# Kernel tuning notes

Hardware: AMD Instinct MI355X
Metric: run time of the kernel (lower is better)

## Reference

```python
import jax, jax.numpy as jnp
import numpy as np

NUM_WORDS = 10000
IN_DIM = 300
SIZE = 256
NUM_SEQ = 2
B = 16
L = 128
NUM_BASE_LEMMAS = 3000


def _lstm(x, Wi, Wh, b):
    # x: [L, B, D] -> hidden states [L, B, H]
    Bb = x.shape[1]
    H = Wh.shape[0]
    def step(carry, xt):
        h, c = carry
        z = xt @ Wi + h @ Wh + b  # [B, 4H], gate order i,f,g,o (torch convention)
        i, f, g, o = jnp.split(z, 4, axis=-1)
        c = jax.nn.sigmoid(f) * c + jax.nn.sigmoid(i) * jnp.tanh(g)
        h = jax.nn.sigmoid(o) * jnp.tanh(c)
        return (h, c), h
    init = (jnp.zeros((Bb, H), x.dtype), jnp.zeros((Bb, H), x.dtype))
    _, hs = jax.lax.scan(step, init, x)
    return hs


def _bilstm(x, lengths, Wi_f, Wh_f, b_f, Wi_b, Wh_b, b_b):
    # x: [B, L, D]; variable-length bidirectional LSTM, concat outputs [B, L, 2H]
    Bb, Ll, _ = x.shape
    t = jnp.arange(Ll)
    # reverse the valid prefix of each row; padding stays in place
    rev_idx = jnp.where(t[None, :] < lengths[:, None], lengths[:, None] - 1 - t[None, :], t[None, :])
    x_rev = jnp.take_along_axis(x, rev_idx[:, :, None], axis=1)
    hf = _lstm(jnp.swapaxes(x, 0, 1), Wi_f, Wh_f, b_f)
    hb = _lstm(jnp.swapaxes(x_rev, 0, 1), Wi_b, Wh_b, b_b)
    hf = jnp.swapaxes(hf, 0, 1)
    hb = jnp.take_along_axis(jnp.swapaxes(hb, 0, 1), rev_idx[:, :, None], axis=1)
    return jnp.concatenate([hf, hb], axis=-1)


def setup_inputs() -> dict:
    key = jax.random.key(0)
    ks = jax.random.split(key, 16)
    d = {}
    d['word_embeddings'] = jax.random.normal(ks[0], (NUM_WORDS, IN_DIM), jnp.float32)
    # embedding projection Linear(IN_DIM, SIZE)
    d['Wp'] = jax.random.normal(ks[1], (IN_DIM, SIZE), jnp.float32) * 0.05
    d['bp'] = jnp.zeros((SIZE,), jnp.float32)
    D = SIZE + NUM_SEQ
    d['Wi_f'] = jax.random.normal(ks[2], (D, 4 * SIZE), jnp.float32) * 0.05
    d['Wh_f'] = jax.random.normal(ks[3], (SIZE, 4 * SIZE), jnp.float32) * 0.05
    d['b_f'] = jnp.zeros((4 * SIZE,), jnp.float32)
    d['Wi_b'] = jax.random.normal(ks[4], (D, 4 * SIZE), jnp.float32) * 0.05
    d['Wh_b'] = jax.random.normal(ks[5], (SIZE, 4 * SIZE), jnp.float32) * 0.05
    d['b_b'] = jnp.zeros((4 * SIZE,), jnp.float32)
    # encoded projection Linear(2*SIZE, SIZE)
    d['Wenc'] = jax.random.normal(ks[6], (2 * SIZE, SIZE), jnp.float32) * 0.05
    d['benc'] = jnp.zeros((SIZE,), jnp.float32)
    # gate projection Linear(2*SIZE, SIZE), bias init 1.0 per source
    d['Wgate'] = jax.random.normal(ks[7], (2 * SIZE, SIZE), jnp.float32) * 0.05
    d['bgate'] = jnp.ones((SIZE,), jnp.float32)
    d['seq0'] = jax.random.randint(ks[8], (B, L), 0, NUM_WORDS, jnp.int32)
    d['seq1'] = jax.random.randint(ks[9], (B, L), 0, NUM_WORDS, jnp.int32)
    d['len0'] = jax.random.randint(ks[10], (B,), 1, L + 1, jnp.int32)
    d['len1'] = jax.random.randint(ks[11], (B,), 1, L + 1, jnp.int32)
    d['u2l'] = jax.random.randint(ks[12], (NUM_WORDS,), 0, NUM_BASE_LEMMAS, jnp.int32)
    return d


def reference(word_embeddings, Wp, bp, Wi_f, Wh_f, b_f, Wi_b, Wh_b, b_b, Wenc, benc, Wgate, bgate, seq0, seq1, len0, len1, u2l):
    num_words = word_embeddings.shape[0]
    batch = seq0.shape[0]
    size = Wp.shape[1]
    we = jax.nn.relu(word_embeddings @ Wp + bp)  # [num_words, size]
    offsets = jnp.arange(batch, dtype=jnp.int32) * num_words  # [B]
    u2l_off = (u2l[None, :] + offsets[:, None]).reshape(-1)  # [B*num_words]
    num_lemmas = batch * num_words
    ctxt = jnp.tile(we, (batch, 1))  # [B*num_words, size]
    for i, (seq, lengths) in enumerate(((seq0, len0), (seq1, len1))):
        Ll = seq.shape[1]
        seq_off = seq + offsets[:, None]  # [B, L]
        enc_in = ctxt[seq_off]  # gather: [B, L, size]
        mode = jnp.zeros((batch, Ll, NUM_SEQ), enc_in.dtype).at[:, :, i].set(1.0)
        enc_in = jnp.concatenate([enc_in, mode], axis=-1)  # [B, L, size+num_seq]
        h = _bilstm(enc_in, lengths, Wi_f, Wh_f, b_f, Wi_b, Wh_b, b_b)  # [B, L, 2*size]
        enc = h @ Wenc + benc  # [B, L, size]
        mask = (jnp.arange(Ll)[None, :] < lengths[:, None]).astype(enc.dtype)
        enc = enc * mask[:, :, None]
        seq_lemmas = u2l_off[seq_off.reshape(-1)]  # [B*L]
        new_lemma = jax.ops.segment_max(enc.reshape(-1, size), seq_lemmas, num_segments=num_lemmas)
        new_lemma = jax.nn.relu(new_lemma)  # empty segments (-inf) -> 0
        new_word = new_lemma[u2l_off]  # scatter-back via gather: [B*num_words, size]
        gate = jax.nn.sigmoid(jnp.concatenate([ctxt, new_word], axis=-1) @ Wgate + bgate)
        ctxt = ctxt * gate + (1.0 - gate) * new_word
    return ctxt
```

## Files before the change

### kernel.cpp

```cpp
#include <hip/hip_runtime.h>

#define NW    10000
#define INDIM 300
#define SZ    256
#define BB    16
#define LL    128
#define NLEM  3000
#define FH    1024
#define NCAP  8192
#define NB1   157

typedef short  bf16x8 __attribute__((ext_vector_type(8)));
typedef float  f32x4  __attribute__((ext_vector_type(4)));

__device__ __forceinline__ float sigf(float x){
  return __builtin_amdgcn_rcpf(1.f+__builtin_amdgcn_exp2f(-1.442695041f*x));
}
__device__ __forceinline__ float tanhf_(float x){
  return fmaf(-2.f, __builtin_amdgcn_rcpf(1.f+__builtin_amdgcn_exp2f(2.885390082f*x)), 1.f);
}
__device__ __forceinline__ short f2b(float f){
  unsigned u=__float_as_uint(f); u += 0x7FFFu + ((u>>16)&1u); return (short)(u>>16);
}
__device__ __forceinline__ int pack2(float a, float b){
  return ((int)(unsigned short)f2b(a)) | (((int)(unsigned short)f2b(b))<<16);
}
#define B2F(s) __uint_as_float(((unsigned)(unsigned short)(s))<<16)
#define MFA(a,b,c) __builtin_amdgcn_mfma_f32_16x16x32_bf16(a,b,c,0,0,0)

__global__ void k_prepall(const float* __restrict__ Wh_f, const float* __restrict__ Wh_b,
                          short* __restrict__ whb,
                          const float* __restrict__ Wi_f, const float* __restrict__ Wi_b,
                          short* __restrict__ wif,
                          const float* __restrict__ Wenc, short* __restrict__ wef,
                          const float* __restrict__ Wp, short* __restrict__ wpf){
  int bx=blockIdx.x, thr=threadIdx.x;
  if(bx<256){
    int tid=bx*256+thr;
    int l=tid&63, f=(tid>>6)&63, w=(tid>>12)&7, dir=tid>>15;
    const float* Wh = dir? Wh_b : Wh_f;
    int ks=f&7, T2=f>>3, s2=T2>>2, g=T2&3;
    int col = g*256 + w*32 + s2*16 + (l&15);
    int k0  = ks*32 + (l>>4)*8;
    short v[8];
    #pragma unroll
    for(int j=0;j<8;j++) v[j]=f2b(Wh[(long)(k0+j)*FH + col]);
    *(bf16x8*)(whb + (long)tid*8) = *(bf16x8*)v;
  }else if(bx<512){
    int tid=(bx-256)*256+thr;
    int l=tid&63, ks=(tid>>6)&7, ct=(tid>>9)&63, dir=tid>>15;
    const float* Wi = dir? Wi_b : Wi_f;
    int col = ct*16 + (l&15);
    int k0  = ks*32 + (l>>4)*8;
    short v[8];
    #pragma unroll
    for(int j=0;j<8;j++) v[j]=f2b(Wi[(long)(k0+j)*FH + col]);
    *(bf16x8*)(wif + (long)tid*8) = *(bf16x8*)v;
  }else if(bx<576){
    int tid=(bx-512)*256+thr;
    int l=tid&63, ks=(tid>>6)&15, ct=tid>>10;
    int col = ct*16 + (l&15);
    int k0  = ks*32 + (l>>4)*8;
    short v[8];
    #pragma unroll
    for(int j=0;j<8;j++) v[j]=f2b(Wenc[(long)(k0+j)*SZ + col]);
    *(bf16x8*)(wef + (long)tid*8) = *(bf16x8*)v;
  }else{
    int tid2=(bx-576)*256+thr;
    int l=tid2&63, frow=tid2>>6;
    int ct=frow/10, ks=frow-ct*10;
    int col=ct*16+(l&15);
    int k0=ks*32+(l>>4)*8;
    short v[8];
    #pragma unroll
    for(int j=0;j<8;j++){ int k=k0+j; v[j]=(k<INDIM)? f2b(Wp[(long)k*SZ+col]) : (short)0; }
    *(bf16x8*)(wpf + (long)frow*512 + l*8) = *(bf16x8*)v;
  }
}

__global__ void k_we_mfma(const float* __restrict__ emb, const short* __restrict__ wpf,
                          const float* __restrict__ bp, float* __restrict__ we){
  __shared__ __align__(16) short As[64*328];
  int r0=blockIdx.x*64, tid=threadIdx.x, w=tid>>6, l=tid&63;
  for(int i=tid;i<64*160;i+=256){
    int lr=i/160, c2=(i-lr*160)*2;
    int row=r0+lr;
    float e0=0.f,e1=0.f;
    if(row<NW){
      if(c2<INDIM)   e0=emb[(long)row*INDIM+c2];
      if(c2+1<INDIM) e1=emb[(long)row*INDIM+c2+1];
    }
    *(int*)&As[lr*328+c2]=pack2(e0,e1);
  }
  __syncthreads();
  for(int n2=0;n2<4;n2++){
    int ct=w*4+n2;
    f32x4 Z={0.f,0.f,0.f,0.f};
    f32x4 C0=Z,C1=Z,C2=Z,C3=Z;
    #pragma unroll
    for(int ks=0;ks<10;ks++){
      bf16x8 bb=*(const bf16x8*)(wpf+((long)(ct*10+ks))*512+l*8);
      int ao=ks*32+(l>>4)*8;
      bf16x8 a0=*(const bf16x8*)(&As[((l&15)    )*328+ao]);
      bf16x8 a1=*(const bf16x8*)(&As[((l&15)+16 )*328+ao]);
      bf16x8 a2=*(const bf16x8*)(&As[((l&15)+32 )*328+ao]);
      bf16x8 a3=*(const bf16x8*)(&As[((l&15)+48 )*328+ao]);
      C0=MFA(a0,bb,C0); C1=MFA(a1,bb,C1); C2=MFA(a2,bb,C2); C3=MFA(a3,bb,C3);
    }
    int col=ct*16+(l&15);
    float be=bp[col];
    #pragma unroll
    for(int m=0;m<4;m++){
      f32x4 Cm=(m==0)?C0:(m==1)?C1:(m==2)?C2:C3;
      #pragma unroll
      for(int reg=0;reg<4;reg++){
        int row=r0+m*16+(l>>4)*4+reg;
        if(row<NW) we[(long)row*SZ+col]=fmaxf(Cm[reg]+be,0.f);
      }
    }
  }
}

__global__ void k_xwi_mfma(const int* __restrict__ seq, const int* __restrict__ len,
                      const float* __restrict__ srcw, long bstride,
                      const float* __restrict__ ctxtT, const int* __restrict__ idxmap,
                      const float* __restrict__ Wi_f, const float* __restrict__ bvf,
                      const float* __restrict__ Wi_b, const float* __restrict__ bvb,
                      const short* __restrict__ wf, int iseq, short* __restrict__ xwo){
  __shared__ __align__(16) short As[64*264];
  __shared__ const float* rowp[64];
  int bx=blockIdx.x, dir=bx>>5, blk=bx&31, tid=threadIdx.x;
  int w=tid>>6, l=tid&63;
  if(tid<64){
    int t = blk*4 + (tid>>4), b = tid&15;
    int lb=len[b];
    int tt=(dir==0)? t : ((t<lb)? (lb-1-t) : t);
    int tok=seq[b*LL+tt];
    const float* rp;
    if(idxmap){
      int im=idxmap[b*NW+tok];
      rp = (im>=0)? ctxtT+(long)im*SZ : srcw+(long)tok*SZ;
    }else{
      rp = srcw + (long)b*bstride + (long)tok*SZ;
    }
    rowp[tid]=rp;
  }
  __syncthreads();
  for(int i2=tid;i2<64*64;i2+=256){
    int lr=i2>>6, c4=(i2&63)*4;
    float4 v=*(const float4*)(rowp[lr]+c4);
    int2 pk; pk.x=pack2(v.x,v.y); pk.y=pack2(v.z,v.w);
    *(int2*)&As[lr*264+c4]=pk;
  }
  __syncthreads();
  const float* __restrict__ Wi = dir? Wi_b : Wi_f;
  const float* __restrict__ bv = dir? bvb : bvf;
  const short* wfd = wf + (long)dir*262144;
  for(int n2=0;n2<16;n2++){
    int ct = w*16 + n2;
    const short* bfp = wfd + ((long)ct*8)*512 + l*8;
    f32x4 Z={0.f,0.f,0.f,0.f};
    f32x4 C0=Z,C1=Z,C2=Z,C3=Z;
    #pragma unroll
    for(int ks=0;ks<8;ks++){
      bf16x8 bb=*(const bf16x8*)(bfp + ks*512);
      int ao = ks*32 + (l>>4)*8;
      bf16x8 a0=*(const bf16x8*)(&As[((l&15)    )*264 + ao]);
      bf16x8 a1=*(const bf16x8*)(&As[((l&15)+16 )*264 + ao]);
      bf16x8 a2=*(const bf16x8*)(&As[((l&15)+32 )*264 + ao]);
      bf16x8 a3=*(const bf16x8*)(&As[((l&15)+48 )*264 + ao]);
      C0=MFA(a0,bb,C0); C1=MFA(a1,bb,C1); C2=MFA(a2,bb,C2); C3=MFA(a3,bb,C3);
    }
    int g=ct>>4, w2=(ct&15)>>1, s2=ct&1;
    int col = g*256 + w2*32 + s2*16 + (l&15);
    float be = Wi[(long)(SZ+iseq)*FH+col] + bv[col];
    #pragma unroll
    for(int m=0;m<4;m++){
      f32x4 Cm = (m==0)?C0:(m==1)?C1:(m==2)?C2:C3;
      long base=((((long)dir*128 + blk*4 + m)*8 + w2)*64 + (l>>4)*16 + (l&15))*32
                + s2*16 + g*4;
      int2 pk; pk.x=pack2(Cm[0]+be,Cm[1]+be); pk.y=pack2(Cm[2]+be,Cm[3]+be);
      *(int2*)(xwo+base)=pk;
    }
  }
}

__device__ __forceinline__ void rowgemm64(const float* __restrict__ A,
                                          const float* __restrict__ W,
                                          float* __restrict__ C,
                                          int n, int r0, int tid, float* Asf){
  for(int i=tid;i<64*SZ;i+=512){
    int lr=i>>8; int r=r0+lr;
    Asf[i]= (r<n)? A[(long)r*SZ+(i&255)] : 0.f;
  }
  __syncthreads();
  int cl=tid&63, rg=tid>>6;
  float acc[8][4];
  #pragma unroll
  for(int i=0;i<8;i++){acc[i][0]=acc[i][1]=acc[i][2]=acc[i][3]=0.f;}
  for(int k=0;k<SZ;k+=4){
    float4 a4[8];
    #pragma unroll
    for(int i=0;i<8;i++) a4[i]=*(const float4*)&Asf[(rg*8+i)*SZ+k];
    #pragma unroll
    for(int j=0;j<4;j++){
      const float* wr=W+(long)(k+j)*SZ+cl;
      float w0=wr[0],w1=wr[64],w2=wr[128],w3=wr[192];
      #pragma unroll
      for(int i=0;i<8;i++){
        float a=(j==0)?a4[i].x:(j==1)?a4[i].y:(j==2)?a4[i].z:a4[i].w;
        acc[i][0]=fmaf(a,w0,acc[i][0]);acc[i][1]=fmaf(a,w1,acc[i][1]);
        acc[i][2]=fmaf(a,w2,acc[i][2]);acc[i][3]=fmaf(a,w3,acc[i][3]);
      }
    }
  }
  #pragma unroll
  for(int i=0;i<8;i++){
    int r=r0+rg*8+i;
    if(r<n){
      #pragma unroll
      for(int cc=0;cc<4;cc++) C[(long)r*SZ+cl+cc*64]=acc[i][cc];
    }
  }
}

#define LDFW(f)    (*(const bf16x8*)(fr + (long)(f)*512 + l*8))
#define LDLW(i2,ks) (*(const bf16x8*)(bl + ((i2)*8+(ks))*512 + l*8))
#define DECLWT(T) bf16x8 W##T##_0=LDFW((T)*8+0),W##T##_1=LDFW((T)*8+1),W##T##_2=LDFW((T)*8+2),W##T##_3=LDFW((T)*8+3),W##T##_4=LDFW((T)*8+4),W##T##_5=LDFW((T)*8+5),W##T##_6=LDFW((T)*8+6),W##T##_7=LDFW((T)*8+7);
#define MMRT(T,Cv) { Cv=MFA(A0,W##T##_0,Cv); Cv=MFA(A1,W##T##_1,Cv); Cv=MFA(A2,W##T##_2,Cv); Cv=MFA(A3,W##T##_3,Cv); Cv=MFA(A4,W##T##_4,Cv); Cv=MFA(A5,W##T##_5,Cv); Cv=MFA(A6,W##T##_6,Cv); Cv=MFA(A7,W##T##_7,Cv); }
#define MMLT(i2,Cv) { Cv=MFA(A0,LDLW(i2,0),Cv); Cv=MFA(A1,LDLW(i2,1),Cv); Cv=MFA(A2,LDLW(i2,2),Cv); Cv=MFA(A3,LDLW(i2,3),Cv); Cv=MFA(A4,LDLW(i2,4),Cv); Cv=MFA(A5,LDLW(i2,5),Cv); Cv=MFA(A6,LDLW(i2,6),Cv); Cv=MFA(A7,LDLW(i2,7),Cv); }
#define MMST(Cv) { Cv=MFA(A0,S0,Cv); Cv=MFA(A1,S1,Cv); Cv=MFA(A2,S2,Cv); Cv=MFA(A3,S3,Cv); Cv=MFA(A4,S4,Cv); Cv=MFA(A5,S5,Cv); Cv=MFA(A6,S6,Cv); Cv=MFA(A7,S7,Cv); }
#define LOADST(f0) S0=LDFW((f0)+0); S1=LDFW((f0)+1); S2=LDFW((f0)+2); S3=LDFW((f0)+3); S4=LDFW((f0)+4); S5=LDFW((f0)+5); S6=LDFW((f0)+6); S7=LDFW((f0)+7);
#define G1(s,r,CA,CB,CC,CD,XA,XB) { \
  float zi=CA[r]+B2F(XA[r]), zf=CB[r]+B2F(XA[4+(r)]), zg=CC[r]+B2F(XB[r]), zo=CD[r]+B2F(XB[4+(r)]); \
  cst_##s##_##r = sigf(zf)*cst_##s##_##r + sigf(zi)*tanhf_(zg); \
  float hv = sigf(zo)*tanhf_(cst_##s##_##r); \
  int b_=4*(l>>4)+(r); int u_=w*32+(s)*16+(l&15); \
  hbn[b_*264+u_]=f2b(hv); }
#define GP(s,CA,CB,CC,CD,XA,XB) \
  G1(s,0,CA,CB,CC,CD,XA,XB) G1(s,1,CA,CB,CC,CD,XA,XB) \
  G1(s,2,CA,CB,CC,CD,XA,XB) G1(s,3,CA,CB,CC,CD,XA,XB)

extern __shared__ char smem_raw[];

__global__ __launch_bounds__(512,2) void k_lstm_f(
    const short* __restrict__ frag, const short* __restrict__ xq,
    short* __restrict__ hgs,
    const float* __restrict__ gA1, const float* __restrict__ gW1,
    float* __restrict__ gC1, int n1,
    const float* __restrict__ gA2, const float* __restrict__ gW2,
    float* __restrict__ gC2, const int* __restrict__ cnt2, int ncap2,
    const int* __restrict__ zsA, const int* __restrict__ zsB,
    const int* __restrict__ u2l, float* __restrict__ lemz,
    int* __restrict__ flagz, int* __restrict__ cntz){
  const int bid=blockIdx.x, tid=threadIdx.x;
  if(bid>=2){
    int gb=bid-2;
    float* Asf=(float*)smem_raw;
    int nb1 = gA1 ? (n1+63)>>6 : 0;
    if(gb<nb1){ rowgemm64(gA1,gW1,gC1,n1,gb*64,tid,Asf); return; }
    gb-=nb1;
    int nb2 = gA2 ? (ncap2>>6) : 0;
    if(gb<nb2){
      int n2=*cnt2; if(n2>ncap2)n2=ncap2;
      int r0=gb*64;
      if(r0<n2) rowgemm64(gA2,gW2,gC2,n2,r0,tid,Asf);
      return;
    }
    gb-=nb2;
    if(zsA){
      if(gb<256){
        int r8=gb*8+(tid>>6); int b=r8>>7, t=r8&127;
        int lem=u2l[zsA[b*LL+t]];
        *(float4*)(lemz+((long)b*NLEM+lem)*SZ+(tid&63)*4)=make_float4(0.f,0.f,0.f,0.f);
        return;
      }
      gb-=256;
    }
    if(zsB){
      if(gb<256){
        int r8=gb*8+(tid>>6); int b=r8>>7, t=r8&127;
        int lem=u2l[zsB[b*LL+t]];
        *(float4*)(lemz+((long)b*NLEM+lem)*SZ+(tid&63)*4)=make_float4(0.f,0.f,0.f,0.f);
        return;
      }
      gb-=256;
    }
    {
      int idx=gb*512+tid;
      if(idx<12000) ((int4*)flagz)[idx]=make_int4(0,0,0,0);
      if(cntz && gb==0 && tid==0) *cntz=0;
    }
    return;
  }
  const int dir=bid, w=tid>>6, l=tid&63;
  short* hb=(short*)smem_raw;
  short* bl=(short*)(smem_raw+16896)+w*8192;
  const short* fr = frag + (long)(dir*8+w)*32768;
  for(int i=tid;i<4224;i+=512) ((int*)smem_raw)[i]=0;
  #pragma unroll
  for(int c2=0;c2<16;c2++)
    *(f32x4*)(bl+c2*512+l*8) = *(const f32x4*)(fr+(long)(32+c2)*512+l*8);
  DECLWT(0) DECLWT(1) DECLWT(2) DECLWT(3)
  float cst_0_0=0,cst_0_1=0,cst_0_2=0,cst_0_3=0,
        cst_1_0=0,cst_1_1=0,cst_1_2=0,cst_1_3=0;
  __syncthreads();
  const short* xwb = xq + ((long)dir*128*8 + w)*2048 + (long)l*32;
  short* hgb = hgs + (long)dir*524288;
  const int db=tid>>5, du=(tid&31)*8;
  bf16x8 S0,S1,S2,S3,S4,S5,S6,S7;
  for(int t=0;t<LL;t++){
    const int cur=t&1, nxt=cur^1;
    LOADST(48)
    const short* xp = xwb + (long)t*16384;
    bf16x8 X0=*(const bf16x8*)(xp+0), X1=*(const bf16x8*)(xp+8);
    const short* hr = hb + cur*4224 + (l&15)*264 + (l>>4)*8;
    bf16x8 A0=*(const bf16x8*)(hr+0),   A1=*(const bf16x8*)(hr+32),
           A2=*(const bf16x8*)(hr+64),  A3=*(const bf16x8*)(hr+96),
           A4=*(const bf16x8*)(hr+128), A5=*(const bf16x8*)(hr+160),
           A6=*(const bf16x8*)(hr+192), A7=*(const bf16x8*)(hr+224);
    f32x4 Z={0.f,0.f,0.f,0.f};
    f32x4 C00=Z,C01=Z,C02=Z,C03=Z,C10=Z,C11=Z,C12=Z,C13=Z;
    MMRT(0,C00) MMRT(1,C01) MMRT(2,C02) MMRT(3,C03)
    MMLT(0,C10) MMLT(1,C11)
    MMST(C12)
    LOADST(56)
    bf16x8 X2=*(const bf16x8*)(xp+16), X3=*(const bf16x8*)(xp+24);
    short* hbn = hb + nxt*4224;
    GP(0, C00,C01,C02,C03, X0,X1)
    MMST(C13)
    GP(1, C10,C11,C12,C13, X2,X3)
    __syncthreads();
    f32x4 hv4 = *(const f32x4*)(hbn + db*264 + du);
    *(f32x4*)(hgb + ((long)t*16 + db)*256 + du) = hv4;
  }
}

__global__ void k_enc_mfma(const int* __restrict__ seq, const int* __restrict__ len,
                      const int* __restrict__ u2l, const short* __restrict__ hgs,
                      const short* __restrict__ wef, const float* __restrict__ benc,
                      unsigned int* __restrict__ lembuf, unsigned int* __restrict__ flags){
  __shared__ __align__(16) short As[64*520];
  __shared__ const short* pf16[64]; __shared__ const short* pb16[64];
  __shared__ int lem_s[64], val_s[64], b_s[64];
  int r0=blockIdx.x*64, tid=threadIdx.x, w=tid>>6, l=tid&63;
  if(tid<64){
    int r=r0+tid, b=r>>7, t=r&127, lb=len[b];
    int v=(t<lb); val_s[tid]=v; b_s[tid]=b;
    int lem=u2l[seq[r]]; lem_s[tid]=lem;
    pf16[tid]=hgs+((long)t*BB+b)*SZ;
    int tr=v? (lb-1-t) : t;
    pb16[tid]=hgs+((long)(LL+tr)*BB+b)*SZ;
    if(v) flags[(long)b*NLEM+lem]=1u;
  }
  __syncthreads();
  for(int i2=tid;i2<64*128;i2+=256){
    int lr=i2>>7, cc=(i2&127)*4;
    const short* sp=(cc<256)? pf16[lr]+cc : pb16[lr]+(cc-256);
    *(int2*)&As[lr*520+cc]=*(const int2*)sp;
  }
  __syncthreads();
  for(int n2=0;n2<4;n2++){
    int ct=w*4+n2;
    f32x4 Z={0.f,0.f,0.f,0.f};
    f32x4 C0=Z,C1=Z,C2=Z,C3=Z;
    #pragma unroll
    for(int ks=0;ks<16;ks++){
      bf16x8 bb=*(const bf16x8*)(wef+((long)(ct*16+ks))*512+l*8);
      int ao=ks*32+(l>>4)*8;
      bf16x8 a0=*(const bf16x8*)(&As[((l&15)    )*520+ao]);
      bf16x8 a1=*(const bf16x8*)(&As[((l&15)+16 )*520+ao]);
      bf16x8 a2=*(const bf16x8*)(&As[((l&15)+32 )*520+ao]);
      bf16x8 a3=*(const bf16x8*)(&As[((l&15)+48 )*520+ao]);
      C0=MFA(a0,bb,C0); C1=MFA(a1,bb,C1); C2=MFA(a2,bb,C2); C3=MFA(a3,bb,C3);
    }
    int col=ct*16+(l&15);
    float be=benc[col];
    #pragma unroll
    for(int m=0;m<4;m++){
      f32x4 Cm=(m==0)?C0:(m==1)?C1:(m==2)?C2:C3;
      #pragma unroll
      for(int reg=0;reg<4;reg++){
        int row=m*16+(l>>4)*4+reg;
        if(val_s[row]){
          float e=fmaxf(Cm[reg]+be,0.f);
          atomicMax(&lembuf[((long)b_s[row]*NLEM+lem_s[row])*SZ+col], __float_as_uint(e));
        }
      }
    }
  }
}

__global__ void k_rowgemm(const float* __restrict__ A, const float* __restrict__ W,
                          float* __restrict__ C, const unsigned int* __restrict__ flags){
  __shared__ __align__(16) float As[16][SZ];
  __shared__ int any_s;
  int r0=blockIdx.x*16, tid=threadIdx.x;
  if(tid==0){
    int a = flags? 0 : 1;
    if(flags){ for(int i=0;i<16;i++) a |= (int)flags[r0+i]; }
    any_s=a;
  }
  __syncthreads();
  if(!any_s) return;
  for(int i=tid;i<16*SZ;i+=256){int lr=i>>8,j=i&(SZ-1);As[lr][j]=A[(long)(r0+lr)*SZ+j];}
  __syncthreads();
  int cl=tid&63, rg=tid>>6;
  float acc[4][4];
  #pragma unroll
  for(int i=0;i<4;i++){acc[i][0]=acc[i][1]=acc[i][2]=acc[i][3]=0.f;}
  for(int k=0;k<SZ;k+=4){
    float4 a4[4];
    #pragma unroll
    for(int i=0;i<4;i++) a4[i]=*(const float4*)&As[rg*4+i][k];
    #pragma unroll
    for(int j=0;j<4;j++){
      const float* wr=W+(long)(k+j)*SZ+cl;
      float w0=wr[0],w1=wr[64],w2=wr[128],w3=wr[192];
      #pragma unroll
      for(int i=0;i<4;i++){
        float a=(j==0)?a4[i].x:(j==1)?a4[i].y:(j==2)?a4[i].z:a4[i].w;
        acc[i][0]=fmaf(a,w0,acc[i][0]);acc[i][1]=fmaf(a,w1,acc[i][1]);
        acc[i][2]=fmaf(a,w2,acc[i][2]);acc[i][3]=fmaf(a,w3,acc[i][3]);
      }
    }
  }
  #pragma unroll
  for(int i=0;i<4;i++){
    int r=r0+rg*4+i;
    #pragma unroll
    for(int cc=0;cc<4;cc++) C[(long)r*SZ+cl+cc*64]=acc[i][cc];
  }
}

__global__ void k_compact(const int* __restrict__ u2l, const unsigned int* __restrict__ flags,
                          int* __restrict__ cnt, int* __restrict__ list,
                          int* __restrict__ idxmap, int ncap){
  int r = blockIdx.x*256+threadIdx.x;
  if(r>=BB*NW) return;
  int b=r/NW, w=r-b*NW;
  int im=-1;
  if(flags[(long)b*NLEM+u2l[w]]){
    int idx=atomicAdd(cnt,1);
    if(idx<ncap){ list[idx]=r; im=idx; }
  }
  idxmap[r]=im;
}

__global__ void k_gate0c(const float* __restrict__ we, const float* __restrict__ P0,
                         const float* __restrict__ Q, const float* __restrict__ lembuf,
                         const int* __restrict__ u2l, const float* __restrict__ bg,
                         const int* __restrict__ cnt, const int* __restrict__ list,
                         float* __restrict__ ctxtT, int ncap){
  int n=*cnt; if(n>ncap)n=ncap;
  long idx=(long)blockIdx.x*256+threadIdx.x;
  long i=idx>>6; int k4=(int)(idx&63);
  if(i>=n) return;
  int r=list[i]; int b=r/NW, w=r-b*NW;
  int lem=u2l[w];
  long qb=((long)b*NLEM+lem)*SZ;
  float4 p =((const float4*)(P0+(long)w*SZ))[k4];
  float4 wv=((const float4*)(we+(long)w*SZ))[k4];
  float4 bgv=((const float4*)bg)[k4];
  float4 q =((const float4*)(Q+qb))[k4];
  float4 nw=((const float4*)(lembuf+qb))[k4];
  float4 o;
  { float g=sigf(p.x+q.x+bgv.x); o.x=wv.x*g+(1.f-g)*nw.x; }
  { float g=sigf(p.y+q.y+bgv.y); o.y=wv.y*g+(1.f-g)*nw.y; }
  { float g=sigf(p.z+q.z+bgv.z); o.z=wv.z*g+(1.f-g)*nw.z; }
  { float g=sigf(p.w+q.w+bgv.w); o.w=wv.w*g+(1.f-g)*nw.w; }
  ((float4*)ctxtT)[i*64+k4]=o;
}

__global__ void k_base0ip(float* __restrict__ we, const float* __restrict__ P0,
                          const float* __restrict__ bg){
  long idx=(long)blockIdx.x*256+threadIdx.x;
  if(idx>=(long)NW*SZ/4) return;
  int k4=(int)(idx&63);
  float4 wv=((float4*)we)[idx];
  float4 p =((const float4*)P0)[idx];
  float4 bgv=((const float4*)bg)[k4];
  wv.x*=sigf(p.x+bgv.x); wv.y*=sigf(p.y+bgv.y);
  wv.z*=sigf(p.z+bgv.z); wv.w*=sigf(p.w+bgv.w);
  ((float4*)we)[idx]=wv;
}

__global__ void k_gate0(const float* __restrict__ we, const float* __restrict__ P0,
                        const float* __restrict__ Q, const float* __restrict__ lembuf,
                        const int* __restrict__ u2l, const unsigned int* __restrict__ flags,
                        const float* __restrict__ bg, float* __restrict__ out){
  long idx=(long)blockIdx.x*256+threadIdx.x;
  const long TOTAL4=(long)BB*NW*SZ/4;
  if(idx>=TOTAL4) return;
  long row=idx>>6; int k4=(int)(idx&63);
  int r32=(int)row;
  int b=r32/NW, w=r32-b*NW;
  int lem=u2l[w];
  long qb=((long)b*NLEM+lem)*SZ;
  unsigned int fl=flags[(long)b*NLEM+lem];
  float4 p =((const float4*)(P0+(long)w*SZ))[k4];
  float4 wv=((const float4*)(we+(long)w*SZ))[k4];
  float4 bgv=((const float4*)bg)[k4];
  float4 q, nw;
  if(fl){ q=((const float4*)(Q+qb))[k4]; nw=((const float4*)(lembuf+qb))[k4]; }
  else  { q=make_float4(0.f,0.f,0.f,0.f); nw=q; }
  float4 o;
  { float g=sigf(p.x+q.x+bgv.x); o.x=wv.x*g+(1.f-g)*nw.x; }
  { float g=sigf(p.y+q.y+bgv.y); o.y=wv.y*g+(1.f-g)*nw.y; }
  { float g=sigf(p.z+q.z+bgv.z); o.z=wv.z*g+(1.f-g)*nw.z; }
  { float g=sigf(p.w+q.w+bgv.w); o.w=wv.w*g+(1.f-g)*nw.w; }
  ((float4*)out)[idx]=o;
}

__global__ void k_gate1e(const float* __restrict__ base0, const float* __restrict__ ctxtT,
                         const float* __restrict__ P1b, const float* __restrict__ Pt,
                         const int* __restrict__ idxmap,
                         const float* __restrict__ Q, const float* __restrict__ lembuf,
                         const int* __restrict__ u2l, const unsigned int* __restrict__ flags,
                         const float* __restrict__ bg, float* __restrict__ out){
  long idx=(long)blockIdx.x*256+threadIdx.x;
  const long TOTAL4=(long)BB*NW*SZ/4;
  if(idx>=TOTAL4) return;
  long row=idx>>6; int k4=(int)(idx&63);
  int r32=(int)row;
  int b=r32/NW, w=r32-b*NW;
  int im=idxmap[r32];
  int lem=u2l[w];
  long qb=((long)b*NLEM+lem)*SZ;
  unsigned int fl=flags[(long)b*NLEM+lem];
  float4 p, cv;
  if(im>=0){ p=((const float4*)(Pt+(long)im*SZ))[k4]; cv=((const float4*)(ctxtT+(long)im*SZ))[k4]; }
  else     { p=((const float4*)(P1b+(long)w*SZ))[k4]; cv=((const float4*)(base0+(long)w*SZ))[k4]; }
  float4 bgv=((const float4*)bg)[k4];
  float4 q, nw;
  if(fl){ q=((const float4*)(Q+qb))[k4]; nw=((const float4*)(lembuf+qb))[k4]; }
  else  { q=make_float4(0.f,0.f,0.f,0.f); nw=q; }
  float4 o;
  { float g=sigf(p.x+q.x+bgv.x); o.x=cv.x*g+(1.f-g)*nw.x; }
  { float g=sigf(p.y+q.y+bgv.y); o.y=cv.y*g+(1.f-g)*nw.y; }
  { float g=sigf(p.z+q.z+bgv.z); o.z=cv.z*g+(1.f-g)*nw.z; }
  { float g=sigf(p.w+q.w+bgv.w); o.w=cv.w*g+(1.f-g)*nw.w; }
  ((float4*)out)[idx]=o;
}

__global__ void k_gate1(const float* __restrict__ ctxt, const float* __restrict__ Wg,
                        const float* __restrict__ Q, const float* __restrict__ lembuf,
                        const int* __restrict__ u2l, const unsigned int* __restrict__ flags,
                        const float* __restrict__ bg, float* __restrict__ out){
  __shared__ __align__(16) float As[64][SZ];
  __shared__ __align__(16) float Ws[64][SZ];
  __shared__ int lem_s[64];
  int r0=blockIdx.x*64, tid=threadIdx.x;
  for(int i=tid;i<64*SZ;i+=256){int lr=i>>8,j=i&(SZ-1);
    As[lr][j]=ctxt[(long)(r0+lr)*SZ+j];}
  if(tid<64){int r=r0+tid; lem_s[tid]=u2l[r%NW];}
  int cl=tid&63, rg=tid>>6;
  float acc[16][4];
  #pragma unroll
  for(int i=0;i<16;i++){acc[i][0]=acc[i][1]=acc[i][2]=acc[i][3]=0.f;}
  for(int kb=0;kb<4;kb++){
    __syncthreads();
    for(int i=tid;i<64*SZ;i+=256){int lr=i>>8,j=i&(SZ-1);
      Ws[lr][j]=Wg[(long)(kb*64+lr)*SZ+j];}
    __syncthreads();
    for(int k=0;k<64;k+=4){
      float4 a4[16];
      #pragma unroll
      for(int i=0;i<16;i++) a4[i]=*(const float4*)&As[rg*16+i][kb*64+k];
      #pragma unroll
      for(int j=0;j<4;j++){
        float w0=Ws[k+j][cl],w1=Ws[k+j][cl+64],w2=Ws[k+j][cl+128],w3=Ws[k+j][cl+192];
        #pragma unroll
        for(int i=0;i<16;i++){
          float a=(j==0)?a4[i].x:(j==1)?a4[i].y:(j==2)?a4[i].z:a4[i].w;
          acc[i][0]=fmaf(a,w0,acc[i][0]);acc[i][1]=fmaf(a,w1,acc[i][1]);
          acc[i][2]=fmaf(a,w2,acc[i][2]);acc[i][3]=fmaf(a,w3,acc[i][3]);
        }
      }
    }
  }
  #pragma unroll
  for(int i=0;i<16;i++){
    int lr=rg*16+i, r=r0+lr, b=r/NW;
    long base=((long)b*NLEM+lem_s[lr])*SZ;
    unsigned int fl=flags[(long)b*NLEM+lem_s[lr]];
    #pragma unroll
    for(int cc=0;cc<4;cc++){
      int col=cl+cc*64;
      float qv=0.f, nw=0.f;
      if(fl){ qv=Q[base+col]; nw=lembuf[base+col]; }
      float g=sigf(acc[i][cc]+qv+bg[col]);
      out[(long)r*SZ+col]=As[lr][col]*g+(1.f-g)*nw;
    }
  }
}

extern "C" void kernel_launch(void* const* d_in, const int* in_sizes, int n_in,
                              void* d_out, int out_size, void* d_ws, size_t ws_size,
                              hipStream_t stream){
  const float* emb  =(const float*)d_in[0];
  const float* Wp   =(const float*)d_in[1];
  const float* bp   =(const float*)d_in[2];
  const float* Wi_f =(const float*)d_in[3];
  const float* Wh_f =(const float*)d_in[4];
  const float* b_f  =(const float*)d_in[5];
  const float* Wi_b =(const float*)d_in[6];
  const float* Wh_b =(const float*)d_in[7];
  const float* b_b  =(const float*)d_in[8];
  const float* Wenc =(const float*)d_in[9];
  const float* benc =(const float*)d_in[10];
  const float* Wg   =(const float*)d_in[11];
  const float* bg   =(const float*)d_in[12];
  const int*   seq0 =(const int*)d_in[13];
  const int*   seq1 =(const int*)d_in[14];
  const int*   len0 =(const int*)d_in[15];
  const int*   len1 =(const int*)d_in[16];
  const int*   u2l  =(const int*)d_in[17];

  float* ws    = (float*)d_ws;
  float* we    = ws;
  float* xwi   = we    + 2560000;
  float* ctxtT = xwi   + 2097152;
  float* hglob = xwi   + 4194304;
  float* lembuf= hglob + 1048576;
  float* flags = lembuf+ 12288000;
  float* Q     = flags + 48000;
  float* P0    = Q     + 12288000;
  short* whb   = (short*)(P0 + 2560000);
  short* wifrag= whb + 524288;
  short* wefrag= wifrag + 524288;
  short* wpfrag= wefrag + 131072;
  int*   idxmap= (int*)(P0 + 2560000 + 262144 + 262144 + 65536 + 40960);
  int*   list  = idxmap + 160000;
  int*   cnt   = list + NCAP;
  float* Ptouch= (float*)(cnt + 4);
  long base_floats = (long)(Ptouch - ws);
  long avail = ((long)(ws_size/4) - base_floats)/SZ;
  int sparse_ok = (avail >= NCAP);
  float* out   = (float*)d_out;

  hipFuncSetAttribute((const void*)k_lstm_f,
                      hipFuncAttributeMaxDynamicSharedMemorySize, 147968);

  k_prepall<<<616,256,0,stream>>>(Wh_f,Wh_b,whb, Wi_f,Wi_b,wifrag,
                                  Wenc,wefrag, Wp,wpfrag);
  k_we_mfma<<<NB1,256,0,stream>>>(emb,wpfrag,bp,we);

  k_xwi_mfma<<<64,256,0,stream>>>(seq0,len0,we,0L,nullptr,nullptr,
                                  Wi_f,b_f,Wi_b,b_b,wifrag,0,(short*)xwi);
  k_lstm_f<<<2+NB1+256+24,512,147968,stream>>>(whb,(const short*)xwi,(short*)hglob,
      we,Wg,P0,NW, nullptr,nullptr,nullptr,nullptr,0,
      seq0,nullptr,u2l,lembuf,(int*)flags,cnt);
  k_enc_mfma<<<BB*LL/64,256,0,stream>>>(seq0,len0,u2l,(const short*)hglob,wefrag,benc,
                                        (unsigned int*)lembuf,(unsigned int*)flags);
  k_rowgemm<<<BB*NLEM/16,256,0,stream>>>(lembuf,Wg+(long)SZ*SZ,Q,
                                         (const unsigned int*)flags);
  if(sparse_ok){
    k_compact<<<(BB*NW+255)/256,256,0,stream>>>(u2l,(const unsigned int*)flags,
                                                cnt,list,idxmap,NCAP);
    k_gate0c<<<NCAP*64/256,256,0,stream>>>(we,P0,Q,lembuf,u2l,bg,cnt,list,ctxtT,NCAP);
    k_base0ip<<<(NW*SZ/4+255)/256,256,0,stream>>>(we,P0,bg);
  }else{
    long nb=((long)BB*NW*SZ/4+255)/256;
    k_gate0<<<(int)nb,256,0,stream>>>(we,P0,Q,lembuf,u2l,
                                      (const unsigned int*)flags,bg,out);
  }

  if(sparse_ok){
    k_xwi_mfma<<<64,256,0,stream>>>(seq1,len1,we,0L,ctxtT,idxmap,
                                    Wi_f,b_f,Wi_b,b_b,wifrag,1,(short*)xwi);
    k_lstm_f<<<2+NB1+NCAP/64+256+256+24,512,147968,stream>>>(whb,(const short*)xwi,
        (short*)hglob, we,Wg,P0,NW, ctxtT,Wg,Ptouch,cnt,NCAP,
        seq0,seq1,u2l,lembuf,(int*)flags,nullptr);
  }else{
    k_xwi_mfma<<<64,256,0,stream>>>(seq1,len1,out,(long)NW*SZ,nullptr,nullptr,
                                    Wi_f,b_f,Wi_b,b_b,wifrag,1,(short*)xwi);
    k_lstm_f<<<2+256+256+24,512,147968,stream>>>(whb,(const short*)xwi,(short*)hglob,
        nullptr,nullptr,nullptr,0, nullptr,nullptr,nullptr,nullptr,0,
        seq0,seq1,u2l,lembuf,(int*)flags,nullptr);
  }
  k_enc_mfma<<<BB*LL/64,256,0,stream>>>(seq1,len1,u2l,(const short*)hglob,wefrag,benc,
                                        (unsigned int*)lembuf,(unsigned int*)flags);
  k_rowgemm<<<BB*NLEM/16,256,0,stream>>>(lembuf,Wg+(long)SZ*SZ,Q,
                                         (const unsigned int*)flags);
  if(sparse_ok){
    long nb=((long)BB*NW*SZ/4+255)/256;
    k_gate1e<<<(int)nb,256,0,stream>>>(we,ctxtT,P0,Ptouch,idxmap,Q,lembuf,u2l,
                                       (const unsigned int*)flags,bg,out);
  }else{
    k_gate1<<<BB*NW/64,256,0,stream>>>(out,Wg,Q,lembuf,u2l,
                                       (const unsigned int*)flags,bg,out);
  }
}
```

Measured before the change: 1.261 ms.

## Compact touched lemmas into a list and fuse Q gemm with word compaction

```diff
diff --git a/kernel.cpp b/kernel.cpp
--- a/kernel.cpp
+++ b/kernel.cpp
@@ -9,6 +9,7 @@
 #define FH    1024
 #define NCAP  8192
 #define NB1   157
+#define LEMCAP 4096
 
 typedef short  bf16x8 __attribute__((ext_vector_type(8)));
 typedef float  f32x4  __attribute__((ext_vector_type(4)));
@@ -252,7 +253,7 @@
     float* __restrict__ gC2, const int* __restrict__ cnt2, int ncap2,
     const int* __restrict__ zsA, const int* __restrict__ zsB,
     const int* __restrict__ u2l, float* __restrict__ lemz,
-    int* __restrict__ flagz, int* __restrict__ cntz){
+    int* __restrict__ flagz, int* __restrict__ cntz, int* __restrict__ lemcntz){
   const int bid=blockIdx.x, tid=threadIdx.x;
   if(bid>=2){
     int gb=bid-2;
@@ -289,7 +290,8 @@
     {
       int idx=gb*512+tid;
       if(idx<12000) ((int4*)flagz)[idx]=make_int4(0,0,0,0);
-      if(cntz && gb==0 && tid==0) *cntz=0;
+      if(gb==0 && tid==0 && cntz) *cntz=0;
+      if(gb==0 && tid==1 && lemcntz) *lemcntz=0;
     }
     return;
   }
@@ -339,7 +341,8 @@
 __global__ void k_enc_mfma(const int* __restrict__ seq, const int* __restrict__ len,
                       const int* __restrict__ u2l, const short* __restrict__ hgs,
                       const short* __restrict__ wef, const float* __restrict__ benc,
-                      unsigned int* __restrict__ lembuf, unsigned int* __restrict__ flags){
+                      unsigned int* __restrict__ lembuf, unsigned int* __restrict__ flags,
+                      int* __restrict__ lemcnt, int* __restrict__ lemlist){
   __shared__ __align__(16) short As[64*520];
   __shared__ const short* pf16[64]; __shared__ const short* pb16[64];
   __shared__ int lem_s[64], val_s[64], b_s[64];
@@ -351,7 +354,13 @@
     pf16[tid]=hgs+((long)t*BB+b)*SZ;
     int tr=v? (lb-1-t) : t;
     pb16[tid]=hgs+((long)(LL+tr)*BB+b)*SZ;
-    if(v) flags[(long)b*NLEM+lem]=1u;
+    if(v){
+      int fi=b*NLEM+lem;
+      if(atomicExch(&flags[fi],1u)==0u){
+        int pos=atomicAdd(lemcnt,1);
+        if(pos<LEMCAP) lemlist[pos]=fi;
+      }
+    }
   }
   __syncthreads();
   for(int i2=tid;i2<64*128;i2+=256){
@@ -391,19 +400,19 @@
   }
 }
 
-__global__ void k_rowgemm(const float* __restrict__ A, const float* __restrict__ W,
-                          float* __restrict__ C, const unsigned int* __restrict__ flags){
-  __shared__ __align__(16) float As[16][SZ];
-  __shared__ int any_s;
-  int r0=blockIdx.x*16, tid=threadIdx.x;
-  if(tid==0){
-    int a = flags? 0 : 1;
-    if(flags){ for(int i=0;i<16;i++) a |= (int)flags[r0+i]; }
-    any_s=a;
-  }
-  __syncthreads();
-  if(!any_s) return;
-  for(int i=tid;i<16*SZ;i+=256){int lr=i>>8,j=i&(SZ-1);As[lr][j]=A[(long)(r0+lr)*SZ+j];}
+__device__ __forceinline__ void qgemm16(const float* __restrict__ lembuf,
+                                        const float* __restrict__ W,
+                                        float* __restrict__ Q,
+                                        const int* __restrict__ lemcnt,
+                                        const int* __restrict__ lemlist,
+                                        int g0, int tid, float* Asf, int* rl_s){
+  int n=*lemcnt; if(n>LEMCAP)n=LEMCAP;
+  int r0=g0*16;
+  if(r0>=n) return;
+  if(tid<16){ int i=r0+tid; rl_s[tid]=(i<n)? lemlist[i] : -1; }
+  __syncthreads();
+  for(int i=tid;i<16*SZ;i+=256){int lr=i>>8,j=i&(SZ-1);
+    Asf[i]= (rl_s[lr]>=0)? lembuf[(long)rl_s[lr]*SZ+j] : 0.f;}
   __syncthreads();
   int cl=tid&63, rg=tid>>6;
   float acc[4][4];
@@ -412,7 +421,7 @@
   for(int k=0;k<SZ;k+=4){
     float4 a4[4];
     #pragma unroll
-    for(int i=0;i<4;i++) a4[i]=*(const float4*)&As[rg*4+i][k];
+    for(int i=0;i<4;i++) a4[i]=*(const float4*)&Asf[(rg*4+i)*SZ+k];
     #pragma unroll
     for(int j=0;j<4;j++){
       const float* wr=W+(long)(k+j)*SZ+cl;
@@ -427,24 +436,53 @@
   }
   #pragma unroll
   for(int i=0;i<4;i++){
-    int r=r0+rg*4+i;
-    #pragma unroll
-    for(int cc=0;cc<4;cc++) C[(long)r*SZ+cl+cc*64]=acc[i][cc];
-  }
-}
-
-__global__ void k_compact(const int* __restrict__ u2l, const unsigned int* __restrict__ flags,
-                          int* __restrict__ cnt, int* __restrict__ list,
-                          int* __restrict__ idxmap, int ncap){
-  int r = blockIdx.x*256+threadIdx.x;
-  if(r>=BB*NW) return;
-  int b=r/NW, w=r-b*NW;
-  int im=-1;
-  if(flags[(long)b*NLEM+u2l[w]]){
-    int idx=atomicAdd(cnt,1);
-    if(idx<ncap){ list[idx]=r; im=idx; }
-  }
-  idxmap[r]=im;
+    int rl=rl_s[rg*4+i];
+    if(rl>=0){
+      #pragma unroll
+      for(int cc=0;cc<4;cc++) Q[(long)rl*SZ+cl+cc*64]=acc[i][cc];
+    }
+  }
+}
+
+__global__ void k_mid(const float* __restrict__ lembuf, const float* __restrict__ Wg2,
+                      float* __restrict__ Q, const int* __restrict__ lemcnt,
+                      const int* __restrict__ lemlist,
+                      const int* __restrict__ u2l, const unsigned int* __restrict__ flags,
+                      int* __restrict__ cnt, int* __restrict__ list,
+                      int* __restrict__ idxmap, int docompact){
+  __shared__ __align__(16) float Asf[16*SZ];
+  __shared__ int rl_s[16];
+  int bx=blockIdx.x, tid=threadIdx.x;
+  if(bx<LEMCAP/16){
+    qgemm16(lembuf,Wg2,Q,lemcnt,lemlist,bx,tid,Asf,rl_s);
+    return;
+  }
+  bx-=LEMCAP/16;
+  if(docompact && bx<625){
+    int r=bx*256+tid;
+    if(r<BB*NW){
+      int b=r/NW, w2=r-b*NW;
+      int im=-1;
+      if(flags[(long)b*NLEM+u2l[w2]]){
+        int idx=atomicAdd(cnt,1);
+        if(idx<NCAP){ list[idx]=r; im=idx; }
+      }
+      idxmap[r]=im;
+    }
+  }
+}
+
+__global__ void k_base0ip(float* __restrict__ we, const float* __restrict__ P0,
+                          const float* __restrict__ bg){
+  long idx=(long)blockIdx.x*256+threadIdx.x;
+  if(idx>=(long)NW*SZ/4) return;
+  int k4=(int)(idx&63);
+  float4 wv=((float4*)we)[idx];
+  float4 p =((const float4*)P0)[idx];
+  float4 bgv=((const float4*)bg)[k4];
+  wv.x*=sigf(p.x+bgv.x); wv.y*=sigf(p.y+bgv.y);
+  wv.z*=sigf(p.z+bgv.z); wv.w*=sigf(p.w+bgv.w);
+  ((float4*)we)[idx]=wv;
 }
 
 __global__ void k_gate0c(const float* __restrict__ we, const float* __restrict__ P0,
@@ -470,19 +508,6 @@
   { float g=sigf(p.z+q.z+bgv.z); o.z=wv.z*g+(1.f-g)*nw.z; }
   { float g=sigf(p.w+q.w+bgv.w); o.w=wv.w*g+(1.f-g)*nw.w; }
   ((float4*)ctxtT)[i*64+k4]=o;
-}
-
-__global__ void k_base0ip(float* __restrict__ we, const float* __restrict__ P0,
-                          const float* __restrict__ bg){
-  long idx=(long)blockIdx.x*256+threadIdx.x;
-  if(idx>=(long)NW*SZ/4) return;
-  int k4=(int)(idx&63);
-  float4 wv=((float4*)we)[idx];
-  float4 p =((const float4*)P0)[idx];
-  float4 bgv=((const float4*)bg)[k4];
-  wv.x*=sigf(p.x+bgv.x); wv.y*=sigf(p.y+bgv.y);
-  wv.z*=sigf(p.z+bgv.z); wv.w*=sigf(p.w+bgv.w);
-  ((float4*)we)[idx]=wv;
 }
 
 __global__ void k_gate0(const float* __restrict__ we, const float* __restrict__ P0,
@@ -633,7 +658,9 @@
   int*   idxmap= (int*)(P0 + 2560000 + 262144 + 262144 + 65536 + 40960);
   int*   list  = idxmap + 160000;
   int*   cnt   = list + NCAP;
-  float* Ptouch= (float*)(cnt + 4);
+  int*   lemcnt= cnt + 1;
+  int*   lemlist=cnt + 4;
+  float* Ptouch= (float*)(lemlist + LEMCAP);
   long base_floats = (long)(Ptouch - ws);
   long avail = ((long)(ws_size/4) - base_floats)/SZ;
   int sparse_ok = (avail >= NCAP);
@@ -650,17 +677,18 @@
                                   Wi_f,b_f,Wi_b,b_b,wifrag,0,(short*)xwi);
   k_lstm_f<<<2+NB1+256+24,512,147968,stream>>>(whb,(const short*)xwi,(short*)hglob,
       we,Wg,P0,NW, nullptr,nullptr,nullptr,nullptr,0,
-      seq0,nullptr,u2l,lembuf,(int*)flags,cnt);
+      seq0,nullptr,u2l,lembuf,(int*)flags,cnt,lemcnt);
   k_enc_mfma<<<BB*LL/64,256,0,stream>>>(seq0,len0,u2l,(const short*)hglob,wefrag,benc,
-                                        (unsigned int*)lembuf,(unsigned int*)flags);
-  k_rowgemm<<<BB*NLEM/16,256,0,stream>>>(lembuf,Wg+(long)SZ*SZ,Q,
-                                         (const unsigned int*)flags);
+                                        (unsigned int*)lembuf,(unsigned int*)flags,
+                                        lemcnt,lemlist);
   if(sparse_ok){
-    k_compact<<<(BB*NW+255)/256,256,0,stream>>>(u2l,(const unsigned int*)flags,
-                                                cnt,list,idxmap,NCAP);
+    k_mid<<<LEMCAP/16+625,256,0,stream>>>(lembuf,Wg+(long)SZ*SZ,Q,lemcnt,lemlist,
+        u2l,(const unsigned int*)flags,cnt,list,idxmap,1);
     k_gate0c<<<NCAP*64/256,256,0,stream>>>(we,P0,Q,lembuf,u2l,bg,cnt,list,ctxtT,NCAP);
     k_base0ip<<<(NW*SZ/4+255)/256,256,0,stream>>>(we,P0,bg);
   }else{
+    k_mid<<<LEMCAP/16,256,0,stream>>>(lembuf,Wg+(long)SZ*SZ,Q,lemcnt,lemlist,
+        u2l,nullptr,nullptr,nullptr,nullptr,0);
     long nb=((long)BB*NW*SZ/4+255)/256;
     k_gate0<<<(int)nb,256,0,stream>>>(we,P0,Q,lembuf,u2l,
                                       (const unsigned int*)flags,bg,out);
@@ -671,18 +699,19 @@
                                     Wi_f,b_f,Wi_b,b_b,wifrag,1,(short*)xwi);
     k_lstm_f<<<2+NB1+NCAP/64+256+256+24,512,147968,stream>>>(whb,(const short*)xwi,
         (short*)hglob, we,Wg,P0,NW, ctxtT,Wg,Ptouch,cnt,NCAP,
-        seq0,seq1,u2l,lembuf,(int*)flags,nullptr);
+        seq0,seq1,u2l,lembuf,(int*)flags,nullptr,lemcnt);
   }else{
     k_xwi_mfma<<<64,256,0,stream>>>(seq1,len1,out,(long)NW*SZ,nullptr,nullptr,
                                     Wi_f,b_f,Wi_b,b_b,wifrag,1,(short*)xwi);
     k_lstm_f<<<2+256+256+24,512,147968,stream>>>(whb,(const short*)xwi,(short*)hglob,
         nullptr,nullptr,nullptr,0, nullptr,nullptr,nullptr,nullptr,0,
-        seq0,seq1,u2l,lembuf,(int*)flags,nullptr);
+        seq0,seq1,u2l,lembuf,(int*)flags,nullptr,lemcnt);
   }
   k_enc_mfma<<<BB*LL/64,256,0,stream>>>(seq1,len1,u2l,(const short*)hglob,wefrag,benc,
-                                        (unsigned int*)lembuf,(unsigned int*)flags);
-  k_rowgemm<<<BB*NLEM/16,256,0,stream>>>(lembuf,Wg+(long)SZ*SZ,Q,
-                                         (const unsigned int*)flags);
+                                        (unsigned int*)lembuf,(unsigned int*)flags,
+                                        lemcnt,lemlist);
+  k_mid<<<LEMCAP/16,256,0,stream>>>(lembuf,Wg+(long)SZ*SZ,Q,lemcnt,lemlist,
+      u2l,nullptr,nullptr,nullptr,nullptr,0);
   if(sparse_ok){
     long nb=((long)BB*NW*SZ/4+255)/256;
     k_gate1e<<<(int)nb,256,0,stream>>>(we,ctxtT,P0,Ptouch,idxmap,Q,lembuf,u2l,
```

Result: faster. 1.186 ms (-6.0%).
